# Optimization experiments

Hardware: AMD Instinct MI355X
Metric: run time of the kernel (lower is better)

Reference implementation:

```python
import jax, jax.numpy as jnp
import numpy as np
import math

B, S, D = 4, 2048, 2048
NH, NKV, HD = 16, 4, 128

def setup_inputs() -> dict:
    key = jax.random.key(0)
    ks = jax.random.split(key, 9)
    s = 1.0 / math.sqrt(D)
    return {
        "x": jax.random.normal(ks[0], (B, S, D), dtype=jnp.float32),
        "Wq": jax.random.normal(ks[1], (D, NH * HD), dtype=jnp.float32) * s,
        "bq": jnp.zeros((NH * HD,), dtype=jnp.float32),
        "Wk": jax.random.normal(ks[2], (D, NKV * HD), dtype=jnp.float32) * s,
        "bk": jnp.zeros((NKV * HD,), dtype=jnp.float32),
        "Wv": jax.random.normal(ks[3], (D, NKV * HD), dtype=jnp.float32) * s,
        "bv": jnp.zeros((NKV * HD,), dtype=jnp.float32),
        "Wo": jax.random.normal(ks[4], (D, D), dtype=jnp.float32) * s,
        "bo": jnp.zeros((D,), dtype=jnp.float32),
    }

def reference(x, Wq, bq, Wk, bk, Wv, bv, Wo, bo):
    b, s, _ = x.shape
    group = NH // NKV
    q = (x @ Wq + bq).reshape(b, s, NH, HD).transpose(0, 2, 1, 3)   # [B,NH,S,HD]
    k = (x @ Wk + bk).reshape(b, s, NKV, HD).transpose(0, 2, 1, 3)  # [B,NKV,S,HD]
    v = (x @ Wv + bv).reshape(b, s, NKV, HD).transpose(0, 2, 1, 3)
    # repeat_interleave KV heads to match query heads
    k = jnp.repeat(k, group, axis=1)  # [B,NH,S,HD]
    v = jnp.repeat(v, group, axis=1)
    scores = jnp.einsum("bhqd,bhkd->bhqk", q, k) / math.sqrt(HD)
    causal = jnp.tril(jnp.ones((s, s), dtype=bool))
    scores = jnp.where(causal, scores, -jnp.inf)
    probs = jax.nn.softmax(scores, axis=-1)  # dropout p=0.0 -> identity
    out = jnp.einsum("bhqk,bhkd->bhqd", probs, v)
    out = out.transpose(0, 2, 1, 3).reshape(b, s, NH * HD)
    return out @ Wo + bo
```

## Files before the change

### kernel.cpp

```cpp
#include <hip/hip_runtime.h>
#include <hip/hip_bf16.h>

typedef __attribute__((ext_vector_type(4)))  float f32x4;
typedef __attribute__((ext_vector_type(16))) float f32x16;
typedef __attribute__((ext_vector_type(8)))  short s16x8;
typedef __attribute__((ext_vector_type(4)))  short s16x4;
typedef __attribute__((ext_vector_type(4)))  float fvec4;

__device__ __forceinline__ short f2bf(float f) {
    union { float f; unsigned u; } x; x.f = f;
    unsigned r = x.u + 0x7fffu + ((x.u >> 16) & 1u);
    return (short)(r >> 16);
}

__device__ __forceinline__ short cvtbf(float f) {
    __hip_bfloat16 t = __float2bfloat16(f);
    return *reinterpret_cast<short*>(&t);
}

__device__ __forceinline__ void gload_lds16(const short* g, short* lds) {
    __builtin_amdgcn_global_load_lds(
        (const __attribute__((address_space(1))) void*)g,
        (__attribute__((address_space(3))) void*)lds, 16, 0, 0);
}

__global__ __launch_bounds__(256) void prep(const float* __restrict__ x,
                                            const float* __restrict__ Wq,
                                            const float* __restrict__ Wk,
                                            const float* __restrict__ Wv,
                                            short* __restrict__ Xb,
                                            short* __restrict__ WqT,
                                            short* __restrict__ WkvT) {
    const int bid = blockIdx.x, tid = threadIdx.x;
    if (bid < 8192) {
        size_t i = ((size_t)bid * 256 + tid) * 8;
        fvec4 a = *(const fvec4*)&x[i];
        fvec4 b = *(const fvec4*)&x[i + 4];
        s16x8 o;
        o[0] = f2bf(a[0]); o[1] = f2bf(a[1]); o[2] = f2bf(a[2]); o[3] = f2bf(a[3]);
        o[4] = f2bf(b[0]); o[5] = f2bf(b[1]); o[6] = f2bf(b[2]); o[7] = f2bf(b[3]);
        *(s16x8*)&Xb[i] = o;
        return;
    }
    const float* W; short* Wt; int N, local;
    if (bid < 12288)      { W = Wq; Wt = WqT;                      N = 2048; local = bid - 8192; }
    else if (bid < 13312) { W = Wk; Wt = WkvT;                     N = 512;  local = bid - 12288; }
    else                  { W = Wv; Wt = WkvT + (size_t)512 * 2048; N = 512; local = bid - 13312; }
    __shared__ float tile[32][33];
    const int k0 = (local & 63) * 32, n0 = (local >> 6) * 32;
    const int tx = tid & 31, ty = tid >> 5;
    #pragma unroll
    for (int i = 0; i < 4; ++i) {
        int k = ty + i * 8;
        tile[k][tx] = W[(size_t)(k0 + k) * N + n0 + tx];
    }
    __syncthreads();
    #pragma unroll
    for (int i = 0; i < 4; ++i) {
        int n = ty + i * 8;
        Wt[(size_t)(n0 + n) * 2048 + k0 + tx] = f2bf(tile[tx][n]);
    }
}

__global__ __launch_bounds__(256) void tconv(const float* __restrict__ W,
                                             short* __restrict__ Wt,
                                             int K, int N) {
    __shared__ float tile[32][33];
    const int k0 = blockIdx.x * 32, n0 = blockIdx.y * 32;
    const int tx = threadIdx.x & 31, ty = threadIdx.x >> 5;
    #pragma unroll
    for (int i = 0; i < 4; ++i) {
        int k = ty + i * 8;
        tile[k][tx] = W[(size_t)(k0 + k) * N + n0 + tx];
    }
    __syncthreads();
    #pragma unroll
    for (int i = 0; i < 4; ++i) {
        int n = ty + i * 8;
        Wt[(size_t)(n0 + n) * K + k0 + tx] = f2bf(tile[tx][n]);
    }
}

template<int MODE>
__global__ __launch_bounds__(512, 1) void gemm256(const short* __restrict__ A,
                                                  const short* __restrict__ Bt,
                                                  const float* __restrict__ bias,
                                                  void* __restrict__ Cv,
                                                  int M, int N, int K) {
    __shared__ __align__(16) short As[2][16384];
    __shared__ __align__(16) short Bs[2][16384];
    const int tid = threadIdx.x, lane = tid & 63, w = tid >> 6;
    const int wr = w >> 2, wc = w & 3;
    const int lr = lane & 15, g = lane >> 4;
    const int bid = blockIdx.x;
    const int xcd = bid & 7, ii = bid >> 3;
    const int m0 = (xcd * 4 + (ii & 3)) * 256;
    const int n0 = (ii >> 2) * 256;
    const int r0 = w * 8 + (lane >> 3);
    const int sw = ((lane & 7) ^ ((lane >> 3) & 7)) * 8;
    const int swr = lr & 7;

    const short* ga = A  + (size_t)(m0 + r0) * K + sw;
    const short* gb = Bt + (size_t)(n0 + r0) * K + sw;

    f32x4 acc[8][4] = {};
    const int NT = K >> 6;

#define STAGE256(d, t) do {                                                     \
    const int kk0_ = (t) << 6;                                                  \
    _Pragma("unroll")                                                           \
    for (int it_ = 0; it_ < 4; ++it_) {                                         \
        gload_lds16(ga + (size_t)(it_ * 64) * K + kk0_, &As[d][it_ * 4096 + w * 512]); \
        gload_lds16(gb + (size_t)(it_ * 64) * K + kk0_, &Bs[d][it_ * 4096 + w * 512]); \
    }                                                                           \
} while (0)

    STAGE256(0, 0);

    for (int T = 0; T < NT; ++T) {
        const int d = T & 1;
        if (T + 1 < NT) {
            STAGE256((T + 1) & 1, T + 1);
            asm volatile("s_waitcnt vmcnt(8)" ::: "memory");
        } else {
            asm volatile("s_waitcnt vmcnt(0)" ::: "memory");
        }
        __builtin_amdgcn_s_barrier();
        __builtin_amdgcn_sched_barrier(0);
        s16x8 bf[4][2];
        #pragma unroll
        for (int n = 0; n < 4; ++n)
            #pragma unroll
            for (int kk = 0; kk < 2; ++kk)
                bf[n][kk] = *(const s16x8*)&Bs[d][(wc * 64 + n * 16 + lr) * 64 +
                                                 (((kk << 2) | g) ^ swr) * 8];
        s16x8 afc[2][2];
        #pragma unroll
        for (int mm = 0; mm < 2; ++mm)
            #pragma unroll
            for (int kk = 0; kk < 2; ++kk)
                afc[mm][kk] = *(const s16x8*)&As[d][(wr * 128 + mm * 16 + lr) * 64 +
                                                   (((kk << 2) | g) ^ swr) * 8];
        #pragma unroll
        for (int p = 0; p < 4; ++p) {
            s16x8 afn[2][2];
            if (p < 3) {
                #pragma unroll
                for (int mm = 0; mm < 2; ++mm)
                    #pragma unroll
                    for (int kk = 0; kk < 2; ++kk)
                        afn[mm][kk] = *(const s16x8*)&As[d][(wr * 128 + ((p + 1) * 2 + mm) * 16 + lr) * 64 +
                                                           (((kk << 2) | g) ^ swr) * 8];
            }
            __builtin_amdgcn_s_setprio(1);
            #pragma unroll
            for (int kk = 0; kk < 2; ++kk)
                #pragma unroll
                for (int mm = 0; mm < 2; ++mm)
                    #pragma unroll
                    for (int n = 0; n < 4; ++n)
                        acc[p * 2 + mm][n] = __builtin_amdgcn_mfma_f32_16x16x32_bf16(
                            afc[mm][kk], bf[n][kk], acc[p * 2 + mm][n], 0, 0, 0);
            __builtin_amdgcn_s_setprio(0);
            __builtin_amdgcn_s_barrier();
            if (p < 3) {
                #pragma unroll
                for (int mm = 0; mm < 2; ++mm)
                    #pragma unroll
                    for (int kk = 0; kk < 2; ++kk)
                        afc[mm][kk] = afn[mm][kk];
            }
        }
        __builtin_amdgcn_sched_barrier(0);
    }
    #pragma unroll
    for (int m = 0; m < 8; ++m)
        #pragma unroll
        for (int j = 0; j < 4; ++j) {
            int row = m0 + wr * 128 + m * 16 + g * 4 + j;
            #pragma unroll
            for (int n = 0; n < 4; ++n) {
                int col = n0 + wc * 64 + n * 16 + lr;
                float v = acc[m][n][j] + bias[col];
                if constexpr (MODE == 1) ((short*)Cv)[(size_t)row * N + col] = f2bf(v);
                else                     ((float*)Cv)[(size_t)row * N + col] = v;
            }
        }
#undef STAGE256
}

__global__ __launch_bounds__(512, 1) void gemm256kv(const short* __restrict__ A,
                                                    const short* __restrict__ Bt,
                                                    const float* __restrict__ bias_k,
                                                    const float* __restrict__ bias_v,
                                                    short* __restrict__ Kout,
                                                    short* __restrict__ Vout,
                                                    int K) {
    __shared__ __align__(16) short As[2][16384];
    __shared__ __align__(16) short Bs[2][8192];
    const int tid = threadIdx.x, lane = tid & 63, w = tid >> 6;
    const int wr = w >> 1, wc = w & 1;
    const int lr = lane & 15, g = lane >> 4;
    const int bid = blockIdx.x;
    const int xcd = bid & 7, ii = bid >> 3;
    const int m0 = (xcd * 4 + (ii & 3)) * 256;
    const int n0 = (ii >> 2) * 128;
    const int r0 = w * 8 + (lane >> 3);
    const int sw = ((lane & 7) ^ ((lane >> 3) & 7)) * 8;
    const int swr = lr & 7;

    const short* ga = A  + (size_t)(m0 + r0) * K + sw;
    const short* gb = Bt + (size_t)(n0 + r0) * K + sw;

    f32x4 acc[4][4] = {};
    const int NT = K >> 6;

#define STAGEKV(d, t) do {                                                      \
    const int kk0_ = (t) << 6;                                                  \
    _Pragma("unroll")                                                           \
    for (int it_ = 0; it_ < 4; ++it_)                                           \
        gload_lds16(ga + (size_t)(it_ * 64) * K + kk0_, &As[d][it_ * 4096 + w * 512]); \
    _Pragma("unroll")                                                           \
    for (int it_ = 0; it_ < 2; ++it_)                                           \
        gload_lds16(gb + (size_t)(it_ * 64) * K + kk0_, &Bs[d][it_ * 4096 + w * 512]); \
} while (0)

    STAGEKV(0, 0);

    for (int T = 0; T < NT; ++T) {
        const int d = T & 1;
        if (T + 1 < NT) {
            STAGEKV((T + 1) & 1, T + 1);
            asm volatile("s_waitcnt vmcnt(6)" ::: "memory");
        } else {
            asm volatile("s_waitcnt vmcnt(0)" ::: "memory");
        }
        __builtin_amdgcn_s_barrier();
        __builtin_amdgcn_sched_barrier(0);
        s16x8 bf[4][2];
        #pragma unroll
        for (int n = 0; n < 4; ++n)
            #pragma unroll
            for (int kk = 0; kk < 2; ++kk)
                bf[n][kk] = *(const s16x8*)&Bs[d][(wc * 64 + n * 16 + lr) * 64 +
                                                 (((kk << 2) | g) ^ swr) * 8];
        s16x8 afc[2][2];
        #pragma unroll
        for (int mm = 0; mm < 2; ++mm)
            #pragma unroll
            for (int kk = 0; kk < 2; ++kk)
                afc[mm][kk] = *(const s16x8*)&As[d][(wr * 64 + mm * 16 + lr) * 64 +
                                                   (((kk << 2) | g) ^ swr) * 8];
        #pragma unroll
        for (int p = 0; p < 2; ++p) {
            s16x8 afn[2][2];
            if (p < 1) {
                #pragma unroll
                for (int mm = 0; mm < 2; ++mm)
                    #pragma unroll
                    for (int kk = 0; kk < 2; ++kk)
                        afn[mm][kk] = *(const s16x8*)&As[d][(wr * 64 + (2 + mm) * 16 + lr) * 64 +
                                                           (((kk << 2) | g) ^ swr) * 8];
            }
            __builtin_amdgcn_s_setprio(1);
            #pragma unroll
            for (int kk = 0; kk < 2; ++kk)
                #pragma unroll
                for (int mm = 0; mm < 2; ++mm)
                    #pragma unroll
                    for (int n = 0; n < 4; ++n)
                        acc[p * 2 + mm][n] = __builtin_amdgcn_mfma_f32_16x16x32_bf16(
                            afc[mm][kk], bf[n][kk], acc[p * 2 + mm][n], 0, 0, 0);
            __builtin_amdgcn_s_setprio(0);
            __builtin_amdgcn_s_barrier();
            if (p < 1) {
                #pragma unroll
                for (int mm = 0; mm < 2; ++mm)
                    #pragma unroll
                    for (int kk = 0; kk < 2; ++kk)
                        afc[mm][kk] = afn[mm][kk];
            }
        }
        __builtin_amdgcn_sched_barrier(0);
    }
    if (n0 < 512) {
        #pragma unroll
        for (int m = 0; m < 4; ++m)
            #pragma unroll
            for (int j = 0; j < 4; ++j) {
                int row = m0 + wr * 64 + m * 16 + g * 4 + j;
                #pragma unroll
                for (int n = 0; n < 4; ++n) {
                    int col = n0 + wc * 64 + n * 16 + lr;
                    Kout[(size_t)row * 512 + col] = f2bf(acc[m][n][j] + bias_k[col]);
                }
            }
    } else {
        #pragma unroll
        for (int m = 0; m < 4; ++m)
            #pragma unroll
            for (int n = 0; n < 4; ++n) {
                int vcol = n0 - 512 + wc * 64 + n * 16 + lr;
                int kvh = vcol >> 7, dd = vcol & 127;
                int row0 = m0 + wr * 64 + m * 16 + g * 4;
                int b = row0 >> 11, s0 = row0 & 2047;
                int s0p = (s0 & ~15) | (((s0 >> 2) & 1) << 3) | (((s0 >> 3) & 1) << 2);
                s16x4 o;
                #pragma unroll
                for (int j = 0; j < 4; ++j) o[j] = f2bf(acc[m][n][j] + bias_v[vcol]);
                *(s16x4*)&Vout[(((size_t)b * 4 + kvh) * 128 + dd) * 2048 + s0p] = o;
            }
    }
#undef STAGEKV
}

#define SC2 0.12751743f

__global__ __launch_bounds__(512, 1) void attn_kernel(const short* __restrict__ Q,
                                                      const short* __restrict__ Kg,
                                                      const short* __restrict__ Vtg,
                                                      short* __restrict__ Oa) {
    __shared__ __align__(16) short Klds[2][8192];
    __shared__ __align__(16) short Vlds[2][8192];
    const int tid = threadIdx.x;
    const int lane = tid & 63, w = tid >> 6;
    const int l31 = lane & 31, hi = lane >> 5, e7 = lane & 7;
    const int ve = hi ^ e7;

    const int bid = blockIdx.x;
    const int grp = bid & 15, j = bid >> 4;
    const int b = grp >> 2, kvh = grp & 3;
    const int h = kvh * 4 + (j & 3);
    const int qtp = (j >> 2) & 3, ph = j >> 4;
    const int qt = ph ? (3 - qtp) : (4 + qtp);
    const int qb = qt << 8;

    const int q_min = qb + w * 32;
    const int qg = q_min + l31;
    const size_t qrow = (size_t)b * 2048 + qg;

    s16x8 qf[8];
    #pragma unroll
    for (int c = 0; c < 8; ++c)
        qf[c] = *(const s16x8*)&Q[qrow * 2048 + h * 128 + c * 16 + hi * 8];

    f32x16 oacc[4] = {};
    float m_run = -1e28f, l_run = 0.f;

    const int nt = (qb >> 6) + 4;

    const short* Kbase = Kg + ((size_t)b * 2048) * 512 + kvh * 128;
    const short* Vbase = Vtg + ((size_t)(b * 4 + kvh)) * 128 * 2048;

    const int krow0 = w * 4 + (lane >> 4), kslot = lane & 15;
    const int vrow0 = w * 8 + (lane >> 3), vslot = lane & 7;

#define STAGE(buf, t) do {                                                        \
    const int kv0_ = (t) << 6;                                                    \
    _Pragma("unroll")                                                             \
    for (int s_ = 0; s_ < 2; ++s_) {                                              \
        int kr = s_ * 32 + krow0;                                                 \
        gload_lds16(Kbase + (size_t)(kv0_ + kr) * 512 + (kslot ^ (kr & 7)) * 8,   \
                    &Klds[buf][s_ * 4096 + w * 512]);                             \
        int vr = s_ * 64 + vrow0;                                                 \
        gload_lds16(Vbase + (size_t)vr * 2048 + kv0_ + (vslot ^ (vr & 7)) * 8,    \
                    &Vlds[buf][s_ * 4096 + w * 512]);                             \
    }                                                                             \
} while (0)

    STAGE(0, 0);
    __syncthreads();

    int cur = 0;
    for (int t = 0; t < nt; ++t) {
        if (t + 1 < nt) STAGE(cur ^ 1, t + 1);
        #pragma unroll
        for (int st = 0; st < 2; ++st) {
            const int kvoff = (t << 6) + (st << 5);
            if (kvoff > q_min) break;
            f32x16 s = {};
            const short* kb = &Klds[cur][((st << 5) + l31) * 128];
            __builtin_amdgcn_s_setprio(1);
            #pragma unroll
            for (int c = 0; c < 8; ++c) {
                s16x8 kf = *(const s16x8*)&kb[(((c << 1) ^ ve)) * 8];
                s = __builtin_amdgcn_mfma_f32_32x32x16_bf16(kf, qf[c], s, 0, 0, 0);
            }
            __builtin_amdgcn_s_setprio(0);
            if (kvoff == q_min) {
                #pragma unroll
                for (int r = 0; r < 16; ++r) {
                    const int rw = (r & 3) + 8 * (r >> 2) + 4 * hi;
                    if (rw > l31) s[r] = -1e30f;
                }
            }
            float m01 = fmaxf(s[0], s[1]),   m23 = fmaxf(s[2], s[3]);
            float m45 = fmaxf(s[4], s[5]),   m67 = fmaxf(s[6], s[7]);
            float m89 = fmaxf(s[8], s[9]),   mab = fmaxf(s[10], s[11]);
            float mcd = fmaxf(s[12], s[13]), mef = fmaxf(s[14], s[15]);
            float mA = fmaxf(fmaxf(m01, m23), fmaxf(m45, m67));
            float mB = fmaxf(fmaxf(m89, mab), fmaxf(mcd, mef));
            float pm = fmaxf(mA, mB);
            pm = fmaxf(pm, __shfl_xor(pm, 32));
            if (!__all(pm <= m_run + 90.5f)) {
                float mn = fmaxf(m_run, pm);
                float fs = __builtin_amdgcn_exp2f((m_run - mn) * SC2);
                l_run *= fs;
                #pragma unroll
                for (int dn = 0; dn < 4; ++dn)
                    #pragma unroll
                    for (int r = 0; r < 16; ++r) oacc[dn][r] *= fs;
                m_run = mn;
            }
            const float mb2 = m_run * SC2;
            #pragma unroll
            for (int r = 0; r < 16; ++r)
                s[r] = __builtin_amdgcn_exp2f(fmaf(s[r], SC2, -mb2));
            float s01 = s[0] + s[1],   s23 = s[2] + s[3];
            float s45 = s[4] + s[5],   s67 = s[6] + s[7];
            float s89 = s[8] + s[9],   sab = s[10] + s[11];
            float scd = s[12] + s[13], sef = s[14] + s[15];
            float sAB = ((s01 + s23) + (s45 + s67)) + ((s89 + sab) + (scd + sef));
            l_run += sAB + __shfl_xor(sAB, 32);
            s16x8 pa0, pa1;
            #pragma unroll
            for (int jj = 0; jj < 8; ++jj) { pa0[jj] = cvtbf(s[jj]); pa1[jj] = cvtbf(s[8 + jj]); }
            const short* vb = &Vlds[cur][l31 * 64];
            __builtin_amdgcn_s_setprio(1);
            #pragma unroll
            for (int dn = 0; dn < 4; ++dn) {
                s16x8 vf = *(const s16x8*)&vb[dn * 2048 + (((st << 2) ^ ve)) * 8];
                oacc[dn] = __builtin_amdgcn_mfma_f32_32x32x16_bf16(vf, pa0, oacc[dn], 0, 0, 0);
            }
            #pragma unroll
            for (int dn = 0; dn < 4; ++dn) {
                s16x8 vf = *(const s16x8*)&vb[dn * 2048 + ((((st << 2) | 2) ^ ve)) * 8];
                oacc[dn] = __builtin_amdgcn_mfma_f32_32x32x16_bf16(vf, pa1, oacc[dn], 0, 0, 0);
            }
            __builtin_amdgcn_s_setprio(0);
        }
        __syncthreads();
        cur ^= 1;
    }
    const float inv = 1.0f / l_run;
    const size_t obase = qrow * 2048 + h * 128;
    #pragma unroll
    for (int dn = 0; dn < 4; ++dn)
        #pragma unroll
        for (int u = 0; u < 4; ++u) {
            s16x4 o;
            #pragma unroll
            for (int jj = 0; jj < 4; ++jj) o[jj] = cvtbf(oacc[dn][u * 4 + jj] * inv);
            *(s16x4*)&Oa[obase + dn * 32 + u * 8 + hi * 4] = o;
        }
#undef STAGE
}

extern "C" void kernel_launch(void* const* d_in, const int* in_sizes, int n_in,
                              void* d_out, int out_size, void* d_ws, size_t ws_size,
                              hipStream_t stream) {
    const float* x  = (const float*)d_in[0];
    const float* Wq = (const float*)d_in[1];
    const float* bq = (const float*)d_in[2];
    const float* Wk = (const float*)d_in[3];
    const float* bk = (const float*)d_in[4];
    const float* Wv = (const float*)d_in[5];
    const float* bv = (const float*)d_in[6];
    const float* Wo = (const float*)d_in[7];
    const float* bo = (const float*)d_in[8];
    float* out = (float*)d_out;

    char* ws = (char*)d_ws;
    short* Xb  = (short*)(ws);
    short* Qb  = (short*)(ws + (size_t)33554432);
    short* Kb  = (short*)(ws + (size_t)67108864);
    short* Vt  = (short*)(ws + (size_t)75497472);
    short* WoT = (short*)(ws);
    char* dob = (char*)d_out;
    short* WqT  = (short*)(dob);
    short* WkvT = (short*)(dob + (size_t)8388608);

    const int M = 8192, D = 2048;

    prep<<<dim3(14336), 256, 0, stream>>>(x, Wq, Wk, Wv, Xb, WqT, WkvT);

    gemm256<1><<<dim3(256), 512, 0, stream>>>(Xb, WqT, bq, Qb, M, 2048, D);
    gemm256kv<<<dim3(256), 512, 0, stream>>>(Xb, WkvT, bk, bv, Kb, Vt, D);

    tconv<<<dim3(64, 64), 256, 0, stream>>>(Wo, WoT, D, D);

    attn_kernel<<<dim3(512), 512, 0, stream>>>(Qb, Kb, Vt, Qb);

    gemm256<0><<<dim3(256), 512, 0, stream>>>(Qb, WoT, bo, out, M, 2048, D);
}
```

Baseline: 331.1 us.

## Restructure attention into 128-row blocks with single-buffered K and split QK/PV phases

The attention kernel now runs 1024 blocks of 256 threads, each covering 128 query rows instead of 256, and drops the paired query-tile ordering. K is single-buffered and prefetched only after both 32-row QK^T products are computed, so the next K load overlaps the softmax and PV work. V stays double-buffered. The GEMM kernels also drop register double-buffering of A fragments and load them directly each sub-step, which lowers register pressure at the cost of less load/MFMA overlap. Smaller blocks raise occupancy and help load balance, but they add more barriers per tile and remove the previous causal work pairing.

```diff
diff --git a/kernel.cpp b/kernel.cpp
--- a/kernel.cpp
+++ b/kernel.cpp
@@ -134,24 +134,15 @@
             for (int kk = 0; kk < 2; ++kk)
                 bf[n][kk] = *(const s16x8*)&Bs[d][(wc * 64 + n * 16 + lr) * 64 +
                                                  (((kk << 2) | g) ^ swr) * 8];
-        s16x8 afc[2][2];
-        #pragma unroll
-        for (int mm = 0; mm < 2; ++mm)
-            #pragma unroll
-            for (int kk = 0; kk < 2; ++kk)
-                afc[mm][kk] = *(const s16x8*)&As[d][(wr * 128 + mm * 16 + lr) * 64 +
-                                                   (((kk << 2) | g) ^ swr) * 8];
         #pragma unroll
         for (int p = 0; p < 4; ++p) {
-            s16x8 afn[2][2];
-            if (p < 3) {
-                #pragma unroll
-                for (int mm = 0; mm < 2; ++mm)
-                    #pragma unroll
-                    for (int kk = 0; kk < 2; ++kk)
-                        afn[mm][kk] = *(const s16x8*)&As[d][(wr * 128 + ((p + 1) * 2 + mm) * 16 + lr) * 64 +
-                                                           (((kk << 2) | g) ^ swr) * 8];
-            }
+            s16x8 af[2][2];
+            #pragma unroll
+            for (int mm = 0; mm < 2; ++mm)
+                #pragma unroll
+                for (int kk = 0; kk < 2; ++kk)
+                    af[mm][kk] = *(const s16x8*)&As[d][(wr * 128 + (p * 2 + mm) * 16 + lr) * 64 +
+                                                      (((kk << 2) | g) ^ swr) * 8];
             __builtin_amdgcn_s_setprio(1);
             #pragma unroll
             for (int kk = 0; kk < 2; ++kk)
@@ -160,16 +151,9 @@
                     #pragma unroll
                     for (int n = 0; n < 4; ++n)
                         acc[p * 2 + mm][n] = __builtin_amdgcn_mfma_f32_16x16x32_bf16(
-                            afc[mm][kk], bf[n][kk], acc[p * 2 + mm][n], 0, 0, 0);
+                            af[mm][kk], bf[n][kk], acc[p * 2 + mm][n], 0, 0, 0);
             __builtin_amdgcn_s_setprio(0);
             __builtin_amdgcn_s_barrier();
-            if (p < 3) {
-                #pragma unroll
-                for (int mm = 0; mm < 2; ++mm)
-                    #pragma unroll
-                    for (int kk = 0; kk < 2; ++kk)
-                        afc[mm][kk] = afn[mm][kk];
-            }
         }
         __builtin_amdgcn_sched_barrier(0);
     }
@@ -244,24 +228,15 @@
             for (int kk = 0; kk < 2; ++kk)
                 bf[n][kk] = *(const s16x8*)&Bs[d][(wc * 64 + n * 16 + lr) * 64 +
                                                  (((kk << 2) | g) ^ swr) * 8];
-        s16x8 afc[2][2];
-        #pragma unroll
-        for (int mm = 0; mm < 2; ++mm)
-            #pragma unroll
-            for (int kk = 0; kk < 2; ++kk)
-                afc[mm][kk] = *(const s16x8*)&As[d][(wr * 64 + mm * 16 + lr) * 64 +
-                                                   (((kk << 2) | g) ^ swr) * 8];
         #pragma unroll
         for (int p = 0; p < 2; ++p) {
-            s16x8 afn[2][2];
-            if (p < 1) {
-                #pragma unroll
-                for (int mm = 0; mm < 2; ++mm)
-                    #pragma unroll
-                    for (int kk = 0; kk < 2; ++kk)
-                        afn[mm][kk] = *(const s16x8*)&As[d][(wr * 64 + (2 + mm) * 16 + lr) * 64 +
-                                                           (((kk << 2) | g) ^ swr) * 8];
-            }
+            s16x8 af[2][2];
+            #pragma unroll
+            for (int mm = 0; mm < 2; ++mm)
+                #pragma unroll
+                for (int kk = 0; kk < 2; ++kk)
+                    af[mm][kk] = *(const s16x8*)&As[d][(wr * 64 + (p * 2 + mm) * 16 + lr) * 64 +
+                                                      (((kk << 2) | g) ^ swr) * 8];
             __builtin_amdgcn_s_setprio(1);
             #pragma unroll
             for (int kk = 0; kk < 2; ++kk)
@@ -270,16 +245,9 @@
                     #pragma unroll
                     for (int n = 0; n < 4; ++n)
                         acc[p * 2 + mm][n] = __builtin_amdgcn_mfma_f32_16x16x32_bf16(
-                            afc[mm][kk], bf[n][kk], acc[p * 2 + mm][n], 0, 0, 0);
+                            af[mm][kk], bf[n][kk], acc[p * 2 + mm][n], 0, 0, 0);
             __builtin_amdgcn_s_setprio(0);
             __builtin_amdgcn_s_barrier();
-            if (p < 1) {
-                #pragma unroll
-                for (int mm = 0; mm < 2; ++mm)
-                    #pragma unroll
-                    for (int kk = 0; kk < 2; ++kk)
-                        afc[mm][kk] = afn[mm][kk];
-            }
         }
         __builtin_amdgcn_sched_barrier(0);
     }
@@ -316,11 +284,11 @@
 
 #define SC2 0.12751743f
 
-__global__ __launch_bounds__(512, 1) void attn_kernel(const short* __restrict__ Q,
+__global__ __launch_bounds__(256, 1) void attn_kernel(const short* __restrict__ Q,
                                                       const short* __restrict__ Kg,
                                                       const short* __restrict__ Vtg,
                                                       short* __restrict__ Oa) {
-    __shared__ __align__(16) short Klds[2][8192];
+    __shared__ __align__(16) short Klds[8192];
     __shared__ __align__(16) short Vlds[2][8192];
     const int tid = threadIdx.x;
     const int lane = tid & 63, w = tid >> 6;
@@ -331,9 +299,8 @@
     const int grp = bid & 15, j = bid >> 4;
     const int b = grp >> 2, kvh = grp & 3;
     const int h = kvh * 4 + (j & 3);
-    const int qtp = (j >> 2) & 3, ph = j >> 4;
-    const int qt = ph ? (3 - qtp) : (4 + qtp);
-    const int qb = qt << 8;
+    const int qt = 15 - (j >> 2);
+    const int qb = qt << 7;
 
     const int q_min = qb + w * 32;
     const int qg = q_min + l31;
@@ -347,7 +314,7 @@
     f32x16 oacc[4] = {};
     float m_run = -1e28f, l_run = 0.f;
 
-    const int nt = (qb >> 6) + 4;
+    const int nt = (qb >> 6) + 2;
 
     const short* Kbase = Kg + ((size_t)b * 2048) * 512 + kvh * 128;
     const short* Vbase = Vtg + ((size_t)(b * 4 + kvh)) * 128 * 2048;
@@ -355,90 +322,105 @@
     const int krow0 = w * 4 + (lane >> 4), kslot = lane & 15;
     const int vrow0 = w * 8 + (lane >> 3), vslot = lane & 7;
 
-#define STAGE(buf, t) do {                                                        \
+#define STAGE_K(t) do {                                                           \
     const int kv0_ = (t) << 6;                                                    \
     _Pragma("unroll")                                                             \
-    for (int s_ = 0; s_ < 2; ++s_) {                                              \
-        int kr = s_ * 32 + krow0;                                                 \
+    for (int s_ = 0; s_ < 4; ++s_) {                                              \
+        int kr = s_ * 16 + krow0;                                                 \
         gload_lds16(Kbase + (size_t)(kv0_ + kr) * 512 + (kslot ^ (kr & 7)) * 8,   \
-                    &Klds[buf][s_ * 4096 + w * 512]);                             \
-        int vr = s_ * 64 + vrow0;                                                 \
+                    &Klds[s_ * 2048 + w * 512]);                                  \
+    }                                                                             \
+} while (0)
+#define STAGE_V(buf, t) do {                                                      \
+    const int kv0_ = (t) << 6;                                                    \
+    _Pragma("unroll")                                                             \
+    for (int s_ = 0; s_ < 4; ++s_) {                                              \
+        int vr = s_ * 32 + vrow0;                                                 \
         gload_lds16(Vbase + (size_t)vr * 2048 + kv0_ + (vslot ^ (vr & 7)) * 8,    \
-                    &Vlds[buf][s_ * 4096 + w * 512]);                             \
+                    &Vlds[buf][s_ * 2048 + w * 512]);                             \
     }                                                                             \
 } while (0)
 
-    STAGE(0, 0);
+#define SMPV(sv, st, domask) do {                                                 \
+    if (domask) {                                                                 \
+        _Pragma("unroll")                                                         \
+        for (int r = 0; r < 16; ++r) {                                            \
+            const int rw = (r & 3) + 8 * (r >> 2) + 4 * hi;                       \
+            if (rw > l31) sv[r] = -1e30f;                                         \
+        }                                                                         \
+    }                                                                             \
+    float mA = fmaxf(fmaxf(fmaxf(sv[0], sv[1]), fmaxf(sv[2], sv[3])),             \
+                     fmaxf(fmaxf(sv[4], sv[5]), fmaxf(sv[6], sv[7])));            \
+    float mB = fmaxf(fmaxf(fmaxf(sv[8], sv[9]), fmaxf(sv[10], sv[11])),           \
+                     fmaxf(fmaxf(sv[12], sv[13]), fmaxf(sv[14], sv[15])));        \
+    float pm = fmaxf(mA, mB);                                                     \
+    pm = fmaxf(pm, __shfl_xor(pm, 32));                                           \
+    if (!__all(pm <= m_run + 90.5f)) {                                            \
+        float mn = fmaxf(m_run, pm);                                              \
+        float fs = __builtin_amdgcn_exp2f((m_run - mn) * SC2);                    \
+        l_run *= fs;                                                              \
+        _Pragma("unroll")                                                         \
+        for (int dn = 0; dn < 4; ++dn)                                            \
+            _Pragma("unroll")                                                     \
+            for (int r = 0; r < 16; ++r) oacc[dn][r] *= fs;                       \
+        m_run = mn;                                                               \
+    }                                                                             \
+    const float mb2 = m_run * SC2;                                                \
+    _Pragma("unroll")                                                             \
+    for (int r = 0; r < 16; ++r)                                                  \
+        sv[r] = __builtin_amdgcn_exp2f(fmaf(sv[r], SC2, -mb2));                   \
+    float sAB = (((sv[0] + sv[1]) + (sv[2] + sv[3])) +                            \
+                 ((sv[4] + sv[5]) + (sv[6] + sv[7]))) +                           \
+                (((sv[8] + sv[9]) + (sv[10] + sv[11])) +                          \
+                 ((sv[12] + sv[13]) + (sv[14] + sv[15])));                        \
+    l_run += sAB + __shfl_xor(sAB, 32);                                           \
+    s16x8 pa0, pa1;                                                               \
+    _Pragma("unroll")                                                             \
+    for (int jj = 0; jj < 8; ++jj) { pa0[jj] = cvtbf(sv[jj]); pa1[jj] = cvtbf(sv[8 + jj]); } \
+    const short* vb = &Vlds[cur][l31 * 64];                                       \
+    _Pragma("unroll")                                                             \
+    for (int dn = 0; dn < 4; ++dn) {                                              \
+        s16x8 vf = *(const s16x8*)&vb[dn * 2048 + ((((st) << 2) ^ ve)) * 8];      \
+        oacc[dn] = __builtin_amdgcn_mfma_f32_32x32x16_bf16(vf, pa0, oacc[dn], 0, 0, 0); \
+    }                                                                             \
+    _Pragma("unroll")                                                             \
+    for (int dn = 0; dn < 4; ++dn) {                                              \
+        s16x8 vf = *(const s16x8*)&vb[dn * 2048 + (((((st) << 2) | 2) ^ ve)) * 8];\
+        oacc[dn] = __builtin_amdgcn_mfma_f32_32x32x16_bf16(vf, pa1, oacc[dn], 0, 0, 0); \
+    }                                                                             \
+} while (0)
+
+    STAGE_K(0);
+    STAGE_V(0, 0);
     __syncthreads();
 
     int cur = 0;
     for (int t = 0; t < nt; ++t) {
-        if (t + 1 < nt) STAGE(cur ^ 1, t + 1);
-        #pragma unroll
-        for (int st = 0; st < 2; ++st) {
-            const int kvoff = (t << 6) + (st << 5);
-            if (kvoff > q_min) break;
-            f32x16 s = {};
-            const short* kb = &Klds[cur][((st << 5) + l31) * 128];
-            __builtin_amdgcn_s_setprio(1);
+        if (t + 1 < nt) STAGE_V(cur ^ 1, t + 1);
+        const int kv0 = t << 6;
+        const bool w0 = kv0 <= q_min;
+        const bool w1 = kv0 + 32 <= q_min;
+        f32x16 s0 = {}, s1 = {};
+        if (w0) {
+            const short* kb = &Klds[l31 * 128];
             #pragma unroll
             for (int c = 0; c < 8; ++c) {
                 s16x8 kf = *(const s16x8*)&kb[(((c << 1) ^ ve)) * 8];
-                s = __builtin_amdgcn_mfma_f32_32x32x16_bf16(kf, qf[c], s, 0, 0, 0);
+                s0 = __builtin_amdgcn_mfma_f32_32x32x16_bf16(kf, qf[c], s0, 0, 0, 0);
             }
-            __builtin_amdgcn_s_setprio(0);
-            if (kvoff == q_min) {
-                #pragma unroll
-                for (int r = 0; r < 16; ++r) {
-                    const int rw = (r & 3) + 8 * (r >> 2) + 4 * hi;
-                    if (rw > l31) s[r] = -1e30f;
-                }
+        }
+        if (w1) {
+            const short* kb = &Klds[(32 + l31) * 128];
+            #pragma unroll
+            for (int c = 0; c < 8; ++c) {
+                s16x8 kf = *(const s16x8*)&kb[(((c << 1) ^ ve)) * 8];
+                s1 = __builtin_amdgcn_mfma_f32_32x32x16_bf16(kf, qf[c], s1, 0, 0, 0);
             }
-            float m01 = fmaxf(s[0], s[1]),   m23 = fmaxf(s[2], s[3]);
-            float m45 = fmaxf(s[4], s[5]),   m67 = fmaxf(s[6], s[7]);
-            float m89 = fmaxf(s[8], s[9]),   mab = fmaxf(s[10], s[11]);
-            float mcd = fmaxf(s[12], s[13]), mef = fmaxf(s[14], s[15]);
-            float mA = fmaxf(fmaxf(m01, m23), fmaxf(m45, m67));
-            float mB = fmaxf(fmaxf(m89, mab), fmaxf(mcd, mef));
-            float pm = fmaxf(mA, mB);
-            pm = fmaxf(pm, __shfl_xor(pm, 32));
-            if (!__all(pm <= m_run + 90.5f)) {
-                float mn = fmaxf(m_run, pm);
-                float fs = __builtin_amdgcn_exp2f((m_run - mn) * SC2);
-                l_run *= fs;
-                #pragma unroll
-                for (int dn = 0; dn < 4; ++dn)
-                    #pragma unroll
-                    for (int r = 0; r < 16; ++r) oacc[dn][r] *= fs;
-                m_run = mn;
-            }
-            const float mb2 = m_run * SC2;
-            #pragma unroll
-            for (int r = 0; r < 16; ++r)
-                s[r] = __builtin_amdgcn_exp2f(fmaf(s[r], SC2, -mb2));
-            float s01 = s[0] + s[1],   s23 = s[2] + s[3];
-            float s45 = s[4] + s[5],   s67 = s[6] + s[7];
-            float s89 = s[8] + s[9],   sab = s[10] + s[11];
-            float scd = s[12] + s[13], sef = s[14] + s[15];
-            float sAB = ((s01 + s23) + (s45 + s67)) + ((s89 + sab) + (scd + sef));
-            l_run += sAB + __shfl_xor(sAB, 32);
-            s16x8 pa0, pa1;
-            #pragma unroll
-            for (int jj = 0; jj < 8; ++jj) { pa0[jj] = cvtbf(s[jj]); pa1[jj] = cvtbf(s[8 + jj]); }
-            const short* vb = &Vlds[cur][l31 * 64];
-            __builtin_amdgcn_s_setprio(1);
-            #pragma unroll
-            for (int dn = 0; dn < 4; ++dn) {
-                s16x8 vf = *(const s16x8*)&vb[dn * 2048 + (((st << 2) ^ ve)) * 8];
-                oacc[dn] = __builtin_amdgcn_mfma_f32_32x32x16_bf16(vf, pa0, oacc[dn], 0, 0, 0);
-            }
-            #pragma unroll
-            for (int dn = 0; dn < 4; ++dn) {
-                s16x8 vf = *(const s16x8*)&vb[dn * 2048 + ((((st << 2) | 2) ^ ve)) * 8];
-                oacc[dn] = __builtin_amdgcn_mfma_f32_32x32x16_bf16(vf, pa1, oacc[dn], 0, 0, 0);
-            }
-            __builtin_amdgcn_s_setprio(0);
-        }
+        }
+        __syncthreads();
+        if (t + 1 < nt) STAGE_K(t + 1);
+        if (w0) SMPV(s0, 0, (kv0 == q_min));
+        if (w1) SMPV(s1, 1, (kv0 + 32 == q_min));
         __syncthreads();
         cur ^= 1;
     }
@@ -453,7 +435,9 @@
             for (int jj = 0; jj < 4; ++jj) o[jj] = cvtbf(oacc[dn][u * 4 + jj] * inv);
             *(s16x4*)&Oa[obase + dn * 32 + u * 8 + hi * 4] = o;
         }
-#undef STAGE
+#undef STAGE_K
+#undef STAGE_V
+#undef SMPV
 }
 
 extern "C" void kernel_launch(void* const* d_in, const int* in_sizes, int n_in,
@@ -489,7 +473,7 @@
 
     tconv<<<dim3(64, 64), 256, 0, stream>>>(Wo, WoT, D, D);
 
-    attn_kernel<<<dim3(512), 512, 0, stream>>>(Qb, Kb, Vt, Qb);
+    attn_kernel<<<dim3(1024), 256, 0, stream>>>(Qb, Kb, Vt, Qb);
 
     gemm256<0><<<dim3(256), 512, 0, stream>>>(Qb, WoT, bo, out, M, 2048, D);
 }
```

Result: slower. 395.1 us (+19.3%).
